# Kernel tuning notes

Measured on AMD Instinct MI355X. Metric: run time of the kernel, lower is better.

## Reference

```python
import jax, jax.numpy as jnp
import numpy as np

OUT_SIZE = 7
SAMPLE_NUM = 2
FINEST_SCALE = 56.0
STRIDES = (4, 8, 16, 32)
IMG_H, IMG_W = 800.0, 1216.0


def roi_align(feat, rois, out_size, spatial_scale, sr):
    """Vectorized RoIAlign (aligned=False / mmdet legacy semantics).
    feat: [B,C,H,W]; rois: [K,5] (batch_idx, x1, y1, x2, y2). Returns [K,C,out,out]."""
    B, C, H, W = feat.shape
    K = rois.shape[0]
    ft = jnp.transpose(feat, (0, 2, 3, 1))  # [B,H,W,C] for channel-last gathers
    b = rois[:, 0].astype(jnp.int32)
    x1 = rois[:, 1] * spatial_scale
    y1 = rois[:, 2] * spatial_scale
    x2 = rois[:, 3] * spatial_scale
    y2 = rois[:, 4] * spatial_scale
    roi_w = jnp.maximum(x2 - x1, 1.0)
    roi_h = jnp.maximum(y2 - y1, 1.0)
    bin_w = roi_w / out_size
    bin_h = roi_h / out_size
    G = out_size * sr  # sample grid points per spatial dim
    g = (jnp.arange(G, dtype=feat.dtype) + 0.5) / sr  # sub-bin centers in bin units
    ys = y1[:, None] + g[None, :] * bin_h[:, None]  # [K,G]
    xs = x1[:, None] + g[None, :] * bin_w[:, None]  # [K,G]
    # validity (points outside [-1, H]/[-1, W] contribute 0)
    vy = (ys >= -1.0) & (ys <= H)
    vx = (xs >= -1.0) & (xs <= W)
    valid = vy[:, :, None] & vx[:, None, :]  # [K,G,G]
    # clamp into the map, then bilinear interpolate
    ysc = jnp.clip(ys, 0.0, H - 1)
    xsc = jnp.clip(xs, 0.0, W - 1)
    y0 = jnp.floor(ysc)
    x0 = jnp.floor(xsc)
    ly = ysc - y0
    lx = xsc - x0
    y0i = y0.astype(jnp.int32)
    x0i = x0.astype(jnp.int32)

    def gather(yi, xi):  # yi:[K,G], xi:[K,G] -> [K,G,G,C]
        yc = jnp.clip(yi, 0, H - 1)
        xc = jnp.clip(xi, 0, W - 1)
        return ft[b[:, None, None], yc[:, :, None], xc[:, None, :], :]

    wy0 = (1.0 - ly)[:, :, None, None]
    wy1 = ly[:, :, None, None]
    wx0 = (1.0 - lx)[:, None, :, None]
    wx1 = lx[:, None, :, None]
    val = (gather(y0i, x0i) * (wy0 * wx0)
           + gather(y0i, x0i + 1) * (wy0 * wx1)
           + gather(y0i + 1, x0i) * (wy1 * wx0)
           + gather(y0i + 1, x0i + 1) * (wy1 * wx1))  # [K,G,G,C]
    val = val * valid[..., None]
    # average the sr x sr samples in each output bin
    val = val.reshape(K, out_size, sr, out_size, sr, C).mean(axis=(2, 4))
    return jnp.transpose(val, (0, 3, 1, 2))  # [K,C,out,out]


def map_roi_levels(rois, num_levels):
    scale = jnp.sqrt((rois[:, 3] - rois[:, 1] + 1.0) * (rois[:, 4] - rois[:, 2] + 1.0))
    lvl = jnp.floor(jnp.log2(scale / FINEST_SCALE + 1e-6))
    return jnp.clip(lvl, 0, num_levels - 1).astype(jnp.int32)


def setup_inputs() -> dict:
    key = jax.random.key(0)
    ks = jax.random.split(key, 10)
    feat0 = jax.random.normal(ks[0], (2, 256, 200, 304), dtype=jnp.float32)
    feat1 = jax.random.normal(ks[1], (2, 256, 100, 152), dtype=jnp.float32)
    feat2 = jax.random.normal(ks[2], (2, 256, 50, 76), dtype=jnp.float32)
    feat3 = jax.random.normal(ks[3], (2, 256, 25, 38), dtype=jnp.float32)
    K = 1024
    b = jax.random.randint(ks[4], (K,), 0, 2).astype(jnp.float32)
    # log-uniform box sizes in [16, 600] px so all 4 FPN levels are used
    logw = jax.random.uniform(ks[5], (K,), minval=np.log(16.0), maxval=np.log(600.0))
    logh = jax.random.uniform(ks[6], (K,), minval=np.log(16.0), maxval=np.log(600.0))
    w = jnp.exp(logw)
    h = jnp.exp(logh)
    cx = jax.random.uniform(ks[7], (K,), minval=0.0, maxval=IMG_W)
    cy = jax.random.uniform(ks[8], (K,), minval=0.0, maxval=IMG_H)
    x1 = jnp.clip(cx - w / 2, 0.0, IMG_W - 2.0)
    y1 = jnp.clip(cy - h / 2, 0.0, IMG_H - 2.0)
    x2 = jnp.clip(cx + w / 2, x1 + 1.0, IMG_W - 1.0)
    y2 = jnp.clip(cy + h / 2, y1 + 1.0, IMG_H - 1.0)
    rois = jnp.stack([b, x1, y1, x2, y2], axis=1).astype(jnp.float32)
    return {"feat0": feat0, "feat1": feat1, "feat2": feat2, "feat3": feat3, "rois": rois}


def reference(feat0, feat1, feat2, feat3, rois):
    feats = [feat0, feat1, feat2, feat3]
    num_levels = len(feats)
    lvls = map_roi_levels(rois, num_levels)  # [K]
    K = rois.shape[0]
    C = feats[0].shape[1]
    out = jnp.zeros((K, C, OUT_SIZE, OUT_SIZE), dtype=feats[0].dtype)
    for i in range(num_levels):
        pooled = roi_align(feats[i], rois, OUT_SIZE, 1.0 / STRIDES[i], SAMPLE_NUM)
        out = out + jnp.where((lvls == i)[:, None, None, None], pooled, 0.0)
    return out
```

## Files before the change

kernel.cpp:

```cpp
#include <hip/hip_runtime.h>
#include <math.h>


#define OUT_SZ 7
#define NCH 256
#define NBINS 49

struct RoiParam {
    int   lvl;
    int   batch;
    float x1, y1;
    float bw, bh;
    int   H, W;
};

__global__ __launch_bounds__(256)
void roi_param_kernel(const float* __restrict__ rois, int K, RoiParam* __restrict__ p)
{
    int k = blockIdx.x * blockDim.x + threadIdx.x;
    if (k >= K) return;
    float b  = rois[k * 5 + 0];
    float x1 = rois[k * 5 + 1];
    float y1 = rois[k * 5 + 2];
    float x2 = rois[k * 5 + 3];
    float y2 = rois[k * 5 + 4];

    float scale = sqrtf((x2 - x1 + 1.0f) * (y2 - y1 + 1.0f));
    int lvl = (int)floorf(log2f(scale * (1.0f / 56.0f) + 1e-6f));
    lvl = lvl < 0 ? 0 : (lvl > 3 ? 3 : lvl);

    float ss = 1.0f / (float)(4 << lvl);
    float sx1 = x1 * ss, sy1 = y1 * ss;
    float sx2 = x2 * ss, sy2 = y2 * ss;
    float rw = fmaxf(sx2 - sx1, 1.0f);
    float rh = fmaxf(sy2 - sy1, 1.0f);

    RoiParam rp;
    rp.lvl   = lvl;
    rp.batch = (int)b;
    rp.x1 = sx1;
    rp.y1 = sy1;
    rp.bw = rw * (1.0f / OUT_SZ);
    rp.bh = rh * (1.0f / OUT_SZ);
    rp.H  = 800  >> (2 + lvl);
    rp.W  = 1216 >> (2 + lvl);
    p[k] = rp;
}

__global__ __launch_bounds__(256)
void roi_align_kernel(const float* __restrict__ f0, const float* __restrict__ f1,
                      const float* __restrict__ f2, const float* __restrict__ f3,
                      const RoiParam* __restrict__ params,
                      float* __restrict__ out, int total)
{
    int i = blockIdx.x * 256 + threadIdx.x;
    if (i >= total) return;

    int bin = i % NBINS;
    int kc  = i / NBINS;
    int c   = kc % NCH;
    int k   = kc / NCH;
    int oy  = bin / OUT_SZ;
    int ox  = bin % OUT_SZ;

    RoiParam rp = params[k];
    int H = rp.H, W = rp.W;
    float fH = (float)H, fW = (float)W;

    const float* fb = (rp.lvl == 0) ? f0 : (rp.lvl == 1) ? f1 : (rp.lvl == 2) ? f2 : f3;
    const float* fc = fb + (size_t)(rp.batch * NCH + c) * (size_t)(H * W);

    int   y0i[2], y1i[2];
    float wy0[2], wy1[2];
    bool  vy[2];
#pragma unroll
    for (int s = 0; s < 2; ++s) {
        float y = rp.y1 + ((float)(2 * oy + s) + 0.5f) * 0.5f * rp.bh;
        vy[s] = (y >= -1.0f) && (y <= fH);
        float yc = fminf(fmaxf(y, 0.0f), fH - 1.0f);
        float yf = floorf(yc);
        int   y0 = (int)yf;
        float ly = yc - yf;
        y0i[s] = y0;
        y1i[s] = (y0 + 1 < H) ? (y0 + 1) : (H - 1);
        wy1[s] = ly;
        wy0[s] = 1.0f - ly;
    }

    int   x0i[2], x1i[2];
    float wx0[2], wx1[2];
    bool  vx[2];
#pragma unroll
    for (int s = 0; s < 2; ++s) {
        float x = rp.x1 + ((float)(2 * ox + s) + 0.5f) * 0.5f * rp.bw;
        vx[s] = (x >= -1.0f) && (x <= fW);
        float xc = fminf(fmaxf(x, 0.0f), fW - 1.0f);
        float xf = floorf(xc);
        int   x0 = (int)xf;
        float lx = xc - xf;
        x0i[s] = x0;
        x1i[s] = (x0 + 1 < W) ? (x0 + 1) : (W - 1);
        wx1[s] = lx;
        wx0[s] = 1.0f - lx;
    }

    float acc = 0.0f;
#pragma unroll
    for (int sy = 0; sy < 2; ++sy) {
#pragma unroll
        for (int sx = 0; sx < 2; ++sx) {
            if (vy[sy] && vx[sx]) {
                const float* r0 = fc + (size_t)y0i[sy] * W;
                const float* r1 = fc + (size_t)y1i[sy] * W;
                float v00 = r0[x0i[sx]];
                float v01 = r0[x1i[sx]];
                float v10 = r1[x0i[sx]];
                float v11 = r1[x1i[sx]];
                acc += v00 * (wy0[sy] * wx0[sx]) + v01 * (wy0[sy] * wx1[sx])
                     + v10 * (wy1[sy] * wx0[sx]) + v11 * (wy1[sy] * wx1[sx]);
            }
        }
    }
    out[i] = acc * 0.25f;
}

extern "C" void kernel_launch(void* const* d_in, const int* in_sizes, int n_in,
                              void* d_out, int out_size, void* d_ws, size_t ws_size,
                              hipStream_t stream)
{
    const float* f0   = (const float*)d_in[0];
    const float* f1   = (const float*)d_in[1];
    const float* f2   = (const float*)d_in[2];
    const float* f3   = (const float*)d_in[3];
    const float* rois = (const float*)d_in[4];
    float* out = (float*)d_out;

    int K = in_sizes[4] / 5;
    if (K <= 0) return;

    RoiParam* params = (RoiParam*)d_ws;

    int pb = (K + 255) / 256;
    roi_param_kernel<<<pb, 256, 0, stream>>>(rois, K, params);

    int total = K * NCH * NBINS;
    int blocks = (total + 255) / 256;
    roi_align_kernel<<<blocks, 256, 0, stream>>>(f0, f1, f2, f3, params, out, total);
}
```

Measured before the change: 369.4 us.

## Fuse ROI param kernel and stage per-ROI footprint in LDS per channel

Merges the ROI parameter kernel into the main RoIAlign kernel and assigns one block per ROI. For each channel, the block loads the ROI's bounding footprint of the feature map into double-buffered shared memory with a one-channel-ahead register prefetch. Four threads then each compute one sample of a bin from LDS and combine their results with a warp shuffle. This replaces scattered per-thread global gathers with coalesced row loads and reuses each loaded texel across samples. In exchange it serialises all 256 channels inside each block with two barriers per channel, limits grid parallelism to K blocks, and relies on every footprint fitting in the fixed 1536-entry LDS buffer.

```diff
diff --git a/kernel.cpp b/kernel.cpp
--- a/kernel.cpp
+++ b/kernel.cpp
@@ -5,123 +5,139 @@
 #define OUT_SZ 7
 #define NCH 256
 #define NBINS 49
-
-struct RoiParam {
-    int   lvl;
-    int   batch;
-    float x1, y1;
-    float bw, bh;
-    int   H, W;
-};
+#define PF 6
+#define LDS_N 1536
 
 __global__ __launch_bounds__(256)
-void roi_param_kernel(const float* __restrict__ rois, int K, RoiParam* __restrict__ p)
+void roi_align_fused(const float* __restrict__ f0, const float* __restrict__ f1,
+                     const float* __restrict__ f2, const float* __restrict__ f3,
+                     const float* __restrict__ rois,
+                     float* __restrict__ out)
 {
-    int k = blockIdx.x * blockDim.x + threadIdx.x;
-    if (k >= K) return;
-    float b  = rois[k * 5 + 0];
-    float x1 = rois[k * 5 + 1];
-    float y1 = rois[k * 5 + 2];
-    float x2 = rois[k * 5 + 3];
-    float y2 = rois[k * 5 + 4];
+    __shared__ float lds[2][LDS_N];
 
-    float scale = sqrtf((x2 - x1 + 1.0f) * (y2 - y1 + 1.0f));
+    const int k = blockIdx.x;
+    const int t = threadIdx.x;
+
+    float rb   = rois[k * 5 + 0];
+    float rix1 = rois[k * 5 + 1];
+    float riy1 = rois[k * 5 + 2];
+    float rix2 = rois[k * 5 + 3];
+    float riy2 = rois[k * 5 + 4];
+
+    float scale = sqrtf((rix2 - rix1 + 1.0f) * (riy2 - riy1 + 1.0f));
     int lvl = (int)floorf(log2f(scale * (1.0f / 56.0f) + 1e-6f));
     lvl = lvl < 0 ? 0 : (lvl > 3 ? 3 : lvl);
 
     float ss = 1.0f / (float)(4 << lvl);
-    float sx1 = x1 * ss, sy1 = y1 * ss;
-    float sx2 = x2 * ss, sy2 = y2 * ss;
-    float rw = fmaxf(sx2 - sx1, 1.0f);
-    float rh = fmaxf(sy2 - sy1, 1.0f);
+    float x1 = rix1 * ss, y1 = riy1 * ss;
+    float rw = fmaxf(rix2 * ss - x1, 1.0f);
+    float rh = fmaxf(riy2 * ss - y1, 1.0f);
+    float bw = rw * (1.0f / OUT_SZ);
+    float bh = rh * (1.0f / OUT_SZ);
+    const int H = 800  >> (2 + lvl);
+    const int W = 1216 >> (2 + lvl);
+    const float fH = (float)H, fW = (float)W;
 
-    RoiParam rp;
-    rp.lvl   = lvl;
-    rp.batch = (int)b;
-    rp.x1 = sx1;
-    rp.y1 = sy1;
-    rp.bw = rw * (1.0f / OUT_SZ);
-    rp.bh = rh * (1.0f / OUT_SZ);
-    rp.H  = 800  >> (2 + lvl);
-    rp.W  = 1216 >> (2 + lvl);
-    p[k] = rp;
-}
+    const float* fb = (lvl == 0) ? f0 : (lvl == 1) ? f1 : (lvl == 2) ? f2 : f3;
+    const int HW = H * W;
+    const float* base = fb + (size_t)((int)rb * NCH) * (size_t)HW;
 
-__global__ __launch_bounds__(256)
-void roi_align_kernel(const float* __restrict__ f0, const float* __restrict__ f1,
-                      const float* __restrict__ f2, const float* __restrict__ f3,
-                      const RoiParam* __restrict__ params,
-                      float* __restrict__ out, int total)
-{
-    int i = blockIdx.x * 256 + threadIdx.x;
-    if (i >= total) return;
+    float xf0 = fminf(fmaxf(x1 + 0.25f * bw, 0.0f), fW - 1.0f);
+    float xfl = fminf(fmaxf(x1 + 6.75f * bw, 0.0f), fW - 1.0f);
+    int xa = (int)floorf(xf0);
+    int xb = min((int)floorf(xfl) + 1, W - 1);
+    float yf0 = fminf(fmaxf(y1 + 0.25f * bh, 0.0f), fH - 1.0f);
+    float yfl = fminf(fmaxf(y1 + 6.75f * bh, 0.0f), fH - 1.0f);
+    int ya = (int)floorf(yf0);
+    int yb = min((int)floorf(yfl) + 1, H - 1);
 
-    int bin = i % NBINS;
-    int kc  = i / NBINS;
-    int c   = kc % NCH;
-    int k   = kc / NCH;
-    int oy  = bin / OUT_SZ;
-    int ox  = bin % OUT_SZ;
+    int Wse    = xb - xa + 1;
+    int Rows   = yb - ya + 1;
+    int stride = Wse | 1;
+    int S      = Rows * Wse;
 
-    RoiParam rp = params[k];
-    int H = rp.H, W = rp.W;
-    float fH = (float)H, fW = (float)W;
-
-    const float* fb = (rp.lvl == 0) ? f0 : (rp.lvl == 1) ? f1 : (rp.lvl == 2) ? f2 : f3;
-    const float* fc = fb + (size_t)(rp.batch * NCH + c) * (size_t)(H * W);
-
-    int   y0i[2], y1i[2];
-    float wy0[2], wy1[2];
-    bool  vy[2];
+    int goff[PF], loff[PF];
+    bool gv[PF];
 #pragma unroll
-    for (int s = 0; s < 2; ++s) {
-        float y = rp.y1 + ((float)(2 * oy + s) + 0.5f) * 0.5f * rp.bh;
-        vy[s] = (y >= -1.0f) && (y <= fH);
-        float yc = fminf(fmaxf(y, 0.0f), fH - 1.0f);
-        float yf = floorf(yc);
-        int   y0 = (int)yf;
-        float ly = yc - yf;
-        y0i[s] = y0;
-        y1i[s] = (y0 + 1 < H) ? (y0 + 1) : (H - 1);
-        wy1[s] = ly;
-        wy0[s] = 1.0f - ly;
+    for (int i = 0; i < PF; ++i) {
+        int idx = t + 256 * i;
+        gv[i] = idx < S;
+        int idx2 = gv[i] ? idx : 0;
+        int r   = idx2 / Wse;
+        int col = idx2 - r * Wse;
+        goff[i] = (ya + r) * W + xa + col;
+        loff[i] = r * stride + col;
     }
 
-    int   x0i[2], x1i[2];
-    float wx0[2], wx1[2];
-    bool  vx[2];
+    int bin = t >> 2;
+    int s   = t & 3;
+    int sy  = s >> 1;
+    int sx  = s & 1;
+    int oy  = bin / OUT_SZ;
+    int ox  = bin - oy * OUT_SZ;
+
+    float xs  = x1 + ((float)(2 * ox + sx) + 0.5f) * 0.5f * bw;
+    float ysv = y1 + ((float)(2 * oy + sy) + 0.5f) * 0.5f * bh;
+    bool vx = (xs  >= -1.0f) && (xs  <= fW);
+    bool vy = (ysv >= -1.0f) && (ysv <= fH);
+    bool vall = vx && vy;
+
+    float xc = fminf(fmaxf(xs, 0.0f), fW - 1.0f);
+    float yc = fminf(fmaxf(ysv, 0.0f), fH - 1.0f);
+    float xflr = floorf(xc), yflr = floorf(yc);
+    int x0 = (int)xflr, y0 = (int)yflr;
+    float lx = xc - xflr, ly = yc - yflr;
+    int xhi = min(x0 + 1, W - 1);
+    int yhi = min(y0 + 1, H - 1);
+
+    int lcx0 = x0  - xa;
+    int lcx1 = xhi - xa;
+    int lro0 = (y0  - ya) * stride;
+    int lro1 = (yhi - ya) * stride;
+    float w00 = (1.0f - ly) * (1.0f - lx);
+    float w01 = (1.0f - ly) * lx;
+    float w10 = ly * (1.0f - lx);
+    float w11 = ly * lx;
+
+    float pv[PF];
 #pragma unroll
-    for (int s = 0; s < 2; ++s) {
-        float x = rp.x1 + ((float)(2 * ox + s) + 0.5f) * 0.5f * rp.bw;
-        vx[s] = (x >= -1.0f) && (x <= fW);
-        float xc = fminf(fmaxf(x, 0.0f), fW - 1.0f);
-        float xf = floorf(xc);
-        int   x0 = (int)xf;
-        float lx = xc - xf;
-        x0i[s] = x0;
-        x1i[s] = (x0 + 1 < W) ? (x0 + 1) : (W - 1);
-        wx1[s] = lx;
-        wx0[s] = 1.0f - lx;
+    for (int i = 0; i < PF; ++i) pv[i] = gv[i] ? base[goff[i]] : 0.0f;
+#pragma unroll
+    for (int i = 0; i < PF; ++i) if (gv[i]) lds[0][loff[i]] = pv[i];
+    __syncthreads();
+
+    float* outk = out + (size_t)k * (NCH * NBINS);
+    int p = 0;
+
+    for (int c = 0; c < NCH; ++c) {
+        if (c + 1 < NCH) {
+            const float* pn = base + (size_t)(c + 1) * HW;
+#pragma unroll
+            for (int i = 0; i < PF; ++i) pv[i] = gv[i] ? pn[goff[i]] : 0.0f;
+        }
+
+        if (t < 196) {
+            const float* L = lds[p];
+            float v00 = L[lro0 + lcx0];
+            float v01 = L[lro0 + lcx1];
+            float v10 = L[lro1 + lcx0];
+            float v11 = L[lro1 + lcx1];
+            float val = vall ? (v00 * w00 + v01 * w01 + v10 * w10 + v11 * w11)
+                             : 0.0f;
+            val += __shfl_xor(val, 1, 64);
+            val += __shfl_xor(val, 2, 64);
+            if (s == 0) outk[c * NBINS + bin] = val * 0.25f;
+        }
+        __syncthreads();
+
+        if (c + 1 < NCH) {
+#pragma unroll
+            for (int i = 0; i < PF; ++i) if (gv[i]) lds[p ^ 1][loff[i]] = pv[i];
+        }
+        __syncthreads();
+        p ^= 1;
     }
-
-    float acc = 0.0f;
-#pragma unroll
-    for (int sy = 0; sy < 2; ++sy) {
-#pragma unroll
-        for (int sx = 0; sx < 2; ++sx) {
-            if (vy[sy] && vx[sx]) {
-                const float* r0 = fc + (size_t)y0i[sy] * W;
-                const float* r1 = fc + (size_t)y1i[sy] * W;
-                float v00 = r0[x0i[sx]];
-                float v01 = r0[x1i[sx]];
-                float v10 = r1[x0i[sx]];
-                float v11 = r1[x1i[sx]];
-                acc += v00 * (wy0[sy] * wx0[sx]) + v01 * (wy0[sy] * wx1[sx])
-                     + v10 * (wy1[sy] * wx0[sx]) + v11 * (wy1[sy] * wx1[sx]);
-            }
-        }
-    }
-    out[i] = acc * 0.25f;
 }
 
 extern "C" void kernel_launch(void* const* d_in, const int* in_sizes, int n_in,
@@ -138,12 +154,5 @@
     int K = in_sizes[4] / 5;
     if (K <= 0) return;
 
-    RoiParam* params = (RoiParam*)d_ws;
-
-    int pb = (K + 255) / 256;
-    roi_param_kernel<<<pb, 256, 0, stream>>>(rois, K, params);
-
-    int total = K * NCH * NBINS;
-    int blocks = (total + 255) / 256;
-    roi_align_kernel<<<blocks, 256, 0, stream>>>(f0, f1, f2, f3, params, out, total);
+    roi_align_fused<<<K, 256, 0, stream>>>(f0, f1, f2, f3, rois, out);
 }
```

Measured after the change: 469.5 us. +27.1%, slower.
